# Kernel tuning notes

Measured on AMD Instinct MI355X. Metric: run time of the kernel, lower is better.

## Reference

```python
import jax, jax.numpy as jnp
import numpy as np

# Router hyperparameters (from init_kwargs)
E = 64        # num_routed_experts
K = 6         # moe_router_topk
G = 8         # num_expert_groups
TG = 3        # topk_group
ALPHA = 0.001 # aux_loss_alpha
EPG = E // G  # experts per group


def setup_inputs() -> dict:
    key = jax.random.key(0)
    k1, k2 = jax.random.split(key)
    hidden_states = jax.random.normal(k1, (4, 4096, 4096), dtype=jnp.float32)
    # kaiming_uniform-ish scale for the gate weight [E, H]
    bound = 1.0 / np.sqrt(4096)
    weight = jax.random.uniform(k2, (E, 4096), dtype=jnp.float32,
                                minval=-bound, maxval=bound)
    return {"hidden_states": hidden_states, "weight": weight}


def reference(hidden_states, weight):
    B, S, H = hidden_states.shape
    T = B * S
    x = hidden_states.reshape(T, H).astype(jnp.float32)
    # gate GEMM + softmax scoring
    logits = jnp.einsum('th,eh->te', x, weight.astype(jnp.float32))  # [T, E]
    scores = jax.nn.softmax(logits, axis=-1)
    # group-limited greedy: keep only experts in the top-TG groups (by group max)
    group_scores = scores.reshape(T, G, EPG).max(axis=-1)            # [T, G]
    _, group_idx = jax.lax.top_k(group_scores, TG)                   # [T, TG]
    group_mask = jnp.zeros((T, G), scores.dtype).at[
        jnp.arange(T)[:, None], group_idx].set(1.0)                  # [T, G]
    score_mask = jnp.repeat(group_mask, EPG, axis=-1)                # [T, E]
    tmp_scores = jnp.where(score_mask > 0, scores, 0.0)
    topk_weight, topk_idx = jax.lax.top_k(tmp_scores, K)             # [T, K]
    # norm_topk_prob = True and top_k > 1 -> normalize
    topk_weight = topk_weight / (topk_weight.sum(axis=-1, keepdims=True) + 1e-20)
    # sequence-level aux loss (seq_aux=True, training, alpha > 0)
    idx_aux = topk_idx.reshape(B, S * K)                             # [B, S*K]
    ce = jax.vmap(lambda idx: jnp.zeros(E, jnp.float32).at[idx].add(1.0))(idx_aux)
    ce = ce / (S * K / E)                                            # [B, E]
    aux_loss = (ce * scores.reshape(B, S, E).mean(axis=1)).sum(axis=1).mean() * ALPHA
    return topk_idx, topk_weight, aux_loss
```

## Files before the change

### kernel.cpp

```cpp
#include <hip/hip_runtime.h>
#include <math.h>

#define TTOK   16384
#define HDIM   4096
#define ENUM   64
#define KTOP   6
#define GNUM   8
#define TGK    3
#define BBATCH 4
#define SSEQ   4096
#define ALPHAC 0.001f

#define KSPLIT 4
#define KSL    (HDIM / KSPLIT)
#define TM     128
#define BK     64
#define NIT    (KSL / BK)

#define AS3(p) ((__attribute__((address_space(3))) void*)(p))
#define AS1(p) ((const __attribute__((address_space(1))) void*)(p))

typedef float wvec16 __attribute__((ext_vector_type(16)));

__global__ __launch_bounds__(256)
void pack_w(const float* __restrict__ W, float* __restrict__ Wp) {
    const int gid = blockIdx.x * 256 + threadIdx.x;
    const int k4 = gid >> 6, e = gid & 63;
    float4 v = *(const float4*)(W + (size_t)e * HDIM + k4 * 4);
    *(float4*)(Wp + (size_t)gid * 4) = v;
}

__global__ __launch_bounds__(512, 4)
void gate_gemm(const float* __restrict__ X, const float* __restrict__ Wp,
               float* __restrict__ lp) {
    __shared__ __align__(16) float Xs[2][TM * BK];

    const int tid  = threadIdx.x;
    const int w    = __builtin_amdgcn_readfirstlane(tid >> 6);
    const int l    = tid & 63;
    const int lm15 = l & 15;

    const int id    = blockIdx.x;
    const int tile  = id >> 2;
    const int slice = id & 3;
    const int T0    = tile * TM;
    const int k0    = slice * KSL;
    const int E0    = w * 8;

    const int rl = l >> 4;
    const float* gsp[4];
#pragma unroll
    for (int r = 0; r < 4; ++r)
        gsp[r] = X + (size_t)(T0 + w * 16 + r * 4 + rl) * HDIM + k0
               + ((lm15 ^ (r * 4 + rl)) << 2);

#define STAGE(buf_, it_) do {                                                   \
    const size_t go_ = (size_t)(it_) * BK;                                      \
    _Pragma("unroll")                                                           \
    for (int r_ = 0; r_ < 4; ++r_)                                              \
        __builtin_amdgcn_global_load_lds(AS1(gsp[r_] + go_),                    \
            AS3(&Xs[buf_][(w * 16 + r_ * 4) * BK]), 16, 0, 0);                  \
} while (0)

    float acc[2][8];
#pragma unroll
    for (int g = 0; g < 2; ++g)
#pragma unroll
        for (int j = 0; j < 8; ++j) acc[g][j] = 0.f;

    const int k4base = k0 >> 2;

    STAGE(0, 0);

    for (int it = 0; it < NIT; ++it) {
        __syncthreads();
        if (it + 1 < NIT) STAGE((it + 1) & 1, it + 1);

        const float* xb = Xs[it & 1];
        const int k4it  = k4base + it * (BK / 4);

        wvec16 wA[2], wB[2];
        {
            const float* wp = Wp + ((size_t)k4it * ENUM + E0) * 4;
            wA[0] = *(const wvec16*)(wp);
            wB[0] = *(const wvec16*)(wp + 16);
        }
#pragma unroll
        for (int kq = 0; kq < 16; ++kq) {
            const int cur = kq & 1, nxt = cur ^ 1;
            if (kq + 1 < 16) {
                const float* wp = Wp + ((size_t)(k4it + kq + 1) * ENUM + E0) * 4;
                wA[nxt] = *(const wvec16*)(wp);
                wB[nxt] = *(const wvec16*)(wp + 16);
            }
            const int slot = (kq ^ lm15) << 2;
#pragma unroll
            for (int g = 0; g < 2; ++g) {
                const float4 xv = *(const float4*)(xb + (g * 64 + l) * BK + slot);
#pragma unroll
                for (int j = 0; j < 4; ++j) {
                    acc[g][j] = fmaf(xv.x, wA[cur][4 * j + 0], acc[g][j]);
                    acc[g][j] = fmaf(xv.y, wA[cur][4 * j + 1], acc[g][j]);
                    acc[g][j] = fmaf(xv.z, wA[cur][4 * j + 2], acc[g][j]);
                    acc[g][j] = fmaf(xv.w, wA[cur][4 * j + 3], acc[g][j]);
                }
#pragma unroll
                for (int j = 0; j < 4; ++j) {
                    acc[g][4 + j] = fmaf(xv.x, wB[cur][4 * j + 0], acc[g][4 + j]);
                    acc[g][4 + j] = fmaf(xv.y, wB[cur][4 * j + 1], acc[g][4 + j]);
                    acc[g][4 + j] = fmaf(xv.z, wB[cur][4 * j + 2], acc[g][4 + j]);
                    acc[g][4 + j] = fmaf(xv.w, wB[cur][4 * j + 3], acc[g][4 + j]);
                }
            }
        }
    }

    float* dst = lp + (size_t)slice * TTOK * ENUM + (size_t)(T0 + l) * ENUM + E0;
#pragma unroll
    for (int g = 0; g < 2; ++g) {
        float* d = dst + (size_t)g * 64 * ENUM;
        *(float4*)(d + 0) = make_float4(acc[g][0], acc[g][1], acc[g][2], acc[g][3]);
        *(float4*)(d + 4) = make_float4(acc[g][4], acc[g][5], acc[g][6], acc[g][7]);
    }
#undef STAGE
}

#define RTOK 64
__global__ __launch_bounds__(256)
void router_topk(const float* __restrict__ lp,
                 float* __restrict__ out_idx, float* __restrict__ out_w,
                 float* __restrict__ ssum_g, int* __restrict__ cnt_g) {
    __shared__ float Ls[RTOK * 67];
    __shared__ float s_m[RTOK], s_inv[RTOK];
    __shared__ float s_ssum[ENUM];
    __shared__ int   s_cnt[ENUM];

    const int tid = threadIdx.x;
    const int t0  = blockIdx.x * RTOK;
    if (tid < ENUM) { s_cnt[tid] = 0; s_ssum[tid] = 0.f; }

#pragma unroll
    for (int r = 0; r < 4; ++r) {
        const int q  = r * 256 + tid;
        const int t  = q >> 4, c4 = q & 15;
        const size_t base = (size_t)(t0 + t) * ENUM + c4 * 4;
        float4 v = *(const float4*)(lp + base);
#pragma unroll
        for (int h = 1; h < KSPLIT; ++h) {
            float4 u = *(const float4*)(lp + (size_t)h * TTOK * ENUM + base);
            v.x += u.x; v.y += u.y; v.z += u.z; v.w += u.w;
        }
        float* d = Ls + t * 67 + c4 * 4;
        d[0] = v.x; d[1] = v.y; d[2] = v.z; d[3] = v.w;
    }
    __syncthreads();

    if (tid < RTOK) {
        const float* row = Ls + tid * 67;

        float gm[GNUM];
#pragma unroll
        for (int g = 0; g < GNUM; ++g) {
            float mg = row[g * 8];
#pragma unroll
            for (int j = 1; j < 8; ++j) mg = fmaxf(mg, row[g * 8 + j]);
            gm[g] = mg;
        }
        float m = gm[0];
#pragma unroll
        for (int g = 1; g < GNUM; ++g) m = fmaxf(m, gm[g]);

        int selmask = 0;
#pragma unroll
        for (int g = 0; g < GNUM; ++g) {
            int rank = 0;
#pragma unroll
            for (int g2 = 0; g2 < GNUM; ++g2)
                rank += (gm[g2] > gm[g]) || (gm[g2] == gm[g] && g2 < g);
            selmask |= (rank < TGK) << g;
        }

        float v0=-1.f,v1=-1.f,v2=-1.f,v3=-1.f,v4=-1.f,v5=-1.f;
        float i0=0.f,i1=0.f,i2=0.f,i3=0.f,i4=0.f,i5=0.f;
        float s = 0.f;
#pragma unroll
        for (int e = 0; e < ENUM; ++e) {
            const float ex = __expf(row[e] - m);
            s += ex;
            const float cand = ((selmask >> (e >> 3)) & 1) ? ex : -1.0f;
            const float fe = (float)e;
            const bool b0 = cand > v0, b1 = cand > v1, b2 = cand > v2,
                       b3 = cand > v3, b4 = cand > v4, b5 = cand > v5;
            v5 = b4 ? v4 : (b5 ? cand : v5);  i5 = b4 ? i4 : (b5 ? fe : i5);
            v4 = b3 ? v3 : (b4 ? cand : v4);  i4 = b3 ? i3 : (b4 ? fe : i4);
            v3 = b2 ? v2 : (b3 ? cand : v3);  i3 = b2 ? i2 : (b3 ? fe : i3);
            v2 = b1 ? v1 : (b2 ? cand : v2);  i2 = b1 ? i1 : (b2 ? fe : i2);
            v1 = b0 ? v0 : (b1 ? cand : v1);  i1 = b0 ? i0 : (b1 ? fe : i1);
            v0 = b0 ? cand : v0;              i0 = b0 ? fe : i0;
        }
        const float invw = 1.0f / (v0 + v1 + v2 + v3 + v4 + v5);
        const int t = t0 + tid;
        float* oi = out_idx + (size_t)t * KTOP;
        float* ow = out_w   + (size_t)t * KTOP;
        oi[0]=i0; oi[1]=i1; oi[2]=i2; oi[3]=i3; oi[4]=i4; oi[5]=i5;
        ow[0]=v0*invw; ow[1]=v1*invw; ow[2]=v2*invw;
        ow[3]=v3*invw; ow[4]=v4*invw; ow[5]=v5*invw;

        atomicAdd(&s_cnt[(int)i0], 1); atomicAdd(&s_cnt[(int)i1], 1);
        atomicAdd(&s_cnt[(int)i2], 1); atomicAdd(&s_cnt[(int)i3], 1);
        atomicAdd(&s_cnt[(int)i4], 1); atomicAdd(&s_cnt[(int)i5], 1);
        s_m[tid] = m; s_inv[tid] = 1.0f / s;
    }
    __syncthreads();

    {
        const int e = tid & 63, strip = tid >> 6;
        float acc = 0.f;
#pragma unroll
        for (int i = 0; i < RTOK / 4; ++i) {
            const int t = strip * (RTOK / 4) + i;
            acc += __expf(Ls[t * 67 + e] - s_m[t]) * s_inv[t];
        }
        atomicAdd(&s_ssum[e], acc);
    }
    __syncthreads();

    const int b = t0 / SSEQ;
    if (tid < ENUM) {
        atomicAdd(&ssum_g[b * ENUM + tid], s_ssum[tid]);
        atomicAdd(&cnt_g[b * ENUM + tid], s_cnt[tid]);
    }
}

__global__ __launch_bounds__(256)
void aux_loss(const float* __restrict__ ssum_g, const int* __restrict__ cnt_g,
              float* __restrict__ out_aux) {
    const int tid = threadIdx.x;
    float v = (float)cnt_g[tid] * (float)ENUM / ((float)SSEQ * (float)KTOP)
            * (ssum_g[tid] / (float)SSEQ);
#pragma unroll
    for (int off = 32; off; off >>= 1) v += __shfl_xor(v, off);
    __shared__ float red[4];
    if ((tid & 63) == 0) red[tid >> 6] = v;
    __syncthreads();
    if (tid == 0)
        out_aux[0] = (red[0] + red[1] + red[2] + red[3]) * (ALPHAC / (float)BBATCH);
}

extern "C" void kernel_launch(void* const* d_in, const int* in_sizes, int n_in,
                              void* d_out, int out_size, void* d_ws, size_t ws_size,
                              hipStream_t stream) {
    const float* X = (const float*)d_in[0];
    const float* W = (const float*)d_in[1];

    float* out     = (float*)d_out;
    float* out_idx = out;
    float* out_w   = out + (size_t)TTOK * KTOP;
    float* out_aux = out + (size_t)2 * TTOK * KTOP;

    float* lp     = (float*)d_ws;
    float* Wp     = lp + (size_t)KSPLIT * TTOK * ENUM;
    float* ssum_g = Wp + (size_t)HDIM * ENUM;
    int*   cnt_g  = (int*)(ssum_g + BBATCH * ENUM);

    hipMemsetAsync(ssum_g, 0, BBATCH * ENUM * (sizeof(float) + sizeof(int)), stream);

    pack_w<<<(HDIM / 4) * ENUM / 256, 256, 0, stream>>>(W, Wp);
    gate_gemm<<<(TTOK / TM) * KSPLIT, 512, 0, stream>>>(X, Wp, lp);
    router_topk<<<TTOK / RTOK, 256, 0, stream>>>(lp, out_idx, out_w, ssum_g, cnt_g);
    aux_loss<<<1, 256, 0, stream>>>(ssum_g, cnt_g, out_aux);
}
```

Measured before the change: 467.6 us.

## Split gate GEMM over expert halves and stage weights in LDS

The gate GEMM now launches twice as many 256-thread blocks, each computing 32 of the 64 experts for a 128-token tile and K-slice. Weight tiles are staged into shared memory via async global-to-LDS loads alongside the X tile, instead of being read per-wave straight from global memory. This targets latency of the weight reads and raises block-level parallelism. In exchange, each X tile is fetched by two blocks, doubling X traffic unless the cache absorbs it.

New measurement: 458.5 us. About the same (-1.9%).

```diff
diff --git a/kernel.cpp b/kernel.cpp
--- a/kernel.cpp
+++ b/kernel.cpp
@@ -14,13 +14,12 @@
 #define KSPLIT 4
 #define KSL    (HDIM / KSPLIT)
 #define TM     128
+#define TE     32
 #define BK     64
 #define NIT    (KSL / BK)
 
 #define AS3(p) ((__attribute__((address_space(3))) void*)(p))
 #define AS1(p) ((const __attribute__((address_space(1))) void*)(p))
-
-typedef float wvec16 __attribute__((ext_vector_type(16)));
 
 __global__ __launch_bounds__(256)
 void pack_w(const float* __restrict__ W, float* __restrict__ Wp) {
@@ -30,36 +29,46 @@
     *(float4*)(Wp + (size_t)gid * 4) = v;
 }
 
-__global__ __launch_bounds__(512, 4)
+__global__ __launch_bounds__(256, 2)
 void gate_gemm(const float* __restrict__ X, const float* __restrict__ Wp,
                float* __restrict__ lp) {
     __shared__ __align__(16) float Xs[2][TM * BK];
+    __shared__ __align__(16) float Ws[2][16 * TE * 4];
 
     const int tid  = threadIdx.x;
-    const int w    = __builtin_amdgcn_readfirstlane(tid >> 6);
+    const int w    = tid >> 6;
     const int l    = tid & 63;
     const int lm15 = l & 15;
 
     const int id    = blockIdx.x;
-    const int tile  = id >> 2;
+    const int tile  = id >> 3;
+    const int eh    = (id >> 2) & 1;
     const int slice = id & 3;
     const int T0    = tile * TM;
     const int k0    = slice * KSL;
     const int E0    = w * 8;
 
     const int rl = l >> 4;
-    const float* gsp[4];
-#pragma unroll
-    for (int r = 0; r < 4; ++r)
-        gsp[r] = X + (size_t)(T0 + w * 16 + r * 4 + rl) * HDIM + k0
-               + ((lm15 ^ (r * 4 + rl)) << 2);
+    const int tb = w * 4 + rl;
+    const float* gx = X + (size_t)(T0 + tb) * HDIM + k0 + ((lm15 ^ tb) << 2);
+
+    const int ehoff = eh * 128;
 
 #define STAGE(buf_, it_) do {                                                   \
     const size_t go_ = (size_t)(it_) * BK;                                      \
     _Pragma("unroll")                                                           \
-    for (int r_ = 0; r_ < 4; ++r_)                                              \
-        __builtin_amdgcn_global_load_lds(AS1(gsp[r_] + go_),                    \
-            AS3(&Xs[buf_][(w * 16 + r_ * 4) * BK]), 16, 0, 0);                  \
+    for (int r_ = 0; r_ < 8; ++r_)                                              \
+        __builtin_amdgcn_global_load_lds(                                       \
+            AS1(gx + (size_t)r_ * 16 * HDIM + go_),                             \
+            AS3(&Xs[buf_][(r_ * 256 + w * 64 + l) * 4]), 16, 0, 0);             \
+    const int k4s_ = (k0 >> 2) + (it_) * 16;                                    \
+    _Pragma("unroll")                                                           \
+    for (int r_ = 0; r_ < 2; ++r_) {                                            \
+        const int q_ = r_ * 256 + tid;                                          \
+        __builtin_amdgcn_global_load_lds(                                       \
+            AS1(Wp + (size_t)(k4s_ + (q_ >> 5)) * 256 + ehoff + (q_ & 31) * 4), \
+            AS3(&Ws[buf_][q_ * 4]), 16, 0, 0);                                  \
+    }                                                                           \
 } while (0)
 
     float acc[2][8];
@@ -67,8 +76,6 @@
     for (int g = 0; g < 2; ++g)
 #pragma unroll
         for (int j = 0; j < 8; ++j) acc[g][j] = 0.f;
-
-    const int k4base = k0 >> 2;
 
     STAGE(0, 0);
 
@@ -76,46 +83,31 @@
         __syncthreads();
         if (it + 1 < NIT) STAGE((it + 1) & 1, it + 1);
 
-        const float* xb = Xs[it & 1];
-        const int k4it  = k4base + it * (BK / 4);
-
-        wvec16 wA[2], wB[2];
-        {
-            const float* wp = Wp + ((size_t)k4it * ENUM + E0) * 4;
-            wA[0] = *(const wvec16*)(wp);
-            wB[0] = *(const wvec16*)(wp + 16);
-        }
+        const float* xb  = Xs[it & 1];
+        const float* wsb = Ws[it & 1];
 #pragma unroll
         for (int kq = 0; kq < 16; ++kq) {
-            const int cur = kq & 1, nxt = cur ^ 1;
-            if (kq + 1 < 16) {
-                const float* wp = Wp + ((size_t)(k4it + kq + 1) * ENUM + E0) * 4;
-                wA[nxt] = *(const wvec16*)(wp);
-                wB[nxt] = *(const wvec16*)(wp + 16);
-            }
-            const int slot = (kq ^ lm15) << 2;
+            float4 wv[8];
+#pragma unroll
+            for (int j = 0; j < 8; ++j)
+                wv[j] = *(const float4*)(wsb + (kq * TE + E0 + j) * 4);
+            const int so = (kq ^ lm15) << 2;
 #pragma unroll
             for (int g = 0; g < 2; ++g) {
-                const float4 xv = *(const float4*)(xb + (g * 64 + l) * BK + slot);
-#pragma unroll
-                for (int j = 0; j < 4; ++j) {
-                    acc[g][j] = fmaf(xv.x, wA[cur][4 * j + 0], acc[g][j]);
-                    acc[g][j] = fmaf(xv.y, wA[cur][4 * j + 1], acc[g][j]);
-                    acc[g][j] = fmaf(xv.z, wA[cur][4 * j + 2], acc[g][j]);
-                    acc[g][j] = fmaf(xv.w, wA[cur][4 * j + 3], acc[g][j]);
-                }
-#pragma unroll
-                for (int j = 0; j < 4; ++j) {
-                    acc[g][4 + j] = fmaf(xv.x, wB[cur][4 * j + 0], acc[g][4 + j]);
-                    acc[g][4 + j] = fmaf(xv.y, wB[cur][4 * j + 1], acc[g][4 + j]);
-                    acc[g][4 + j] = fmaf(xv.z, wB[cur][4 * j + 2], acc[g][4 + j]);
-                    acc[g][4 + j] = fmaf(xv.w, wB[cur][4 * j + 3], acc[g][4 + j]);
+                const float4 xv = *(const float4*)(xb + (g * 64 + l) * BK + so);
+#pragma unroll
+                for (int j = 0; j < 8; ++j) {
+                    acc[g][j] = fmaf(xv.x, wv[j].x, acc[g][j]);
+                    acc[g][j] = fmaf(xv.y, wv[j].y, acc[g][j]);
+                    acc[g][j] = fmaf(xv.z, wv[j].z, acc[g][j]);
+                    acc[g][j] = fmaf(xv.w, wv[j].w, acc[g][j]);
                 }
             }
         }
     }
 
-    float* dst = lp + (size_t)slice * TTOK * ENUM + (size_t)(T0 + l) * ENUM + E0;
+    float* dst = lp + (size_t)slice * TTOK * ENUM + (size_t)(T0 + l) * ENUM
+               + eh * TE + E0;
 #pragma unroll
     for (int g = 0; g < 2; ++g) {
         float* d = dst + (size_t)g * 64 * ENUM;
@@ -266,7 +258,7 @@
     hipMemsetAsync(ssum_g, 0, BBATCH * ENUM * (sizeof(float) + sizeof(int)), stream);
 
     pack_w<<<(HDIM / 4) * ENUM / 256, 256, 0, stream>>>(W, Wp);
-    gate_gemm<<<(TTOK / TM) * KSPLIT, 512, 0, stream>>>(X, Wp, lp);
+    gate_gemm<<<(TTOK / TM) * 2 * KSPLIT, 256, 0, stream>>>(X, Wp, lp);
     router_topk<<<TTOK / RTOK, 256, 0, stream>>>(lp, out_idx, out_w, ssum_g, cnt_g);
     aux_loss<<<1, 256, 0, stream>>>(ssum_g, cnt_g, out_aux);
 }
```
